# Optimization experiments

Hardware: AMD Instinct MI355X
Metric: run time of the kernel (lower is better)

The kernel has to match this reference:

```python
import jax, jax.numpy as jnp
import numpy as np
from jax import lax

PATCH = 16          # patch_size
LAM = 0.5           # lambda_sparse
TAU = 10.0          # tau
ITERS = 50          # lca_iterations
DT = 0.1            # LCA step size
N_BASES = 256
INPUT_DIM = PATCH * PATCH * 3


def setup_inputs() -> dict:
    key = jax.random.key(0)
    k1, k2 = jax.random.split(key)
    image = jax.random.normal(k1, (64, 3, 224, 224), dtype=jnp.float32)
    D = jax.random.normal(k2, (N_BASES, INPUT_DIM), dtype=jnp.float32)
    D = D / jnp.linalg.norm(D, axis=1, keepdims=True)  # unit-norm bases
    return {"image": image, "dictionary": D, "stride": 8}


def _softshrink(u):
    return jnp.sign(u) * jnp.maximum(jnp.abs(u) - LAM, 0.0)


def reference(image, dictionary, stride):
    n_bases = dictionary.shape[0]
    # extract overlapping patches, feature order (C, ph, pw) matches torch unfold layout
    patches = lax.conv_general_dilated_patches(
        image, (PATCH, PATCH), (stride, stride), 'VALID')  # (B, C*P*P, nh, nw)
    B, D, nh, nw = patches.shape
    patches = patches.transpose(0, 2, 3, 1).reshape(B, nh * nw, D)
    # per-patch standardization (torch .std is unbiased -> ddof=1)
    patches = patches - patches.mean(axis=-1, keepdims=True)
    std = jnp.std(patches, axis=-1, ddof=1, keepdims=True)
    patches = patches / (std + 1e-8)

    pf = patches.reshape(-1, D)  # (B*n_patches, input_dim)
    gram = dictionary @ dictionary.T - jnp.eye(n_bases, dtype=dictionary.dtype)
    b = pf @ dictionary.T        # (N, n_bases) feedforward drive

    def step(u, _):
        a = _softshrink(u)
        du = (b - u - a @ gram) / TAU
        return u + DT * du, None

    u0 = jnp.zeros_like(b)
    u, _ = lax.scan(step, u0, None, length=ITERS)
    codes = _softshrink(u).reshape(B, nh * nw, n_bases)
    return codes.max(axis=1)  # pool='max' -> (B, n_bases)
```

## Files before the change

kernel.cpp:

```cpp
#include <hip/hip_runtime.h>
#include <hip/hip_bf16.h>

#define NB 256
#define IDIM 768
#define NPP 729
#define PSTRIDE 768
#define NIMG 64
#define ITERS 50
#define LN 64
#define LBLK 12

typedef float f32x4 __attribute__((ext_vector_type(4)));
typedef short bf16x8 __attribute__((ext_vector_type(8)));

__device__ __forceinline__ short f2bf(float x) {
  union { float f; unsigned u; } v; v.f = x;
  unsigned r = v.u + 0x7FFFu + ((v.u >> 16) & 1u);
  return (short)(r >> 16);
}

__device__ __forceinline__ unsigned cvt_pk_bf16(float lo, float hi) {
  unsigned r;
  asm("v_cvt_pk_bf16_f32 %0, %1, %2" : "=v"(r) : "v"(lo), "v"(hi));
  return r;
}

__global__ __launch_bounds__(256) void k_cvt(const float* __restrict__ D,
                                             short* __restrict__ Dbf) {
  size_t i = (size_t)(blockIdx.x * 256 + threadIdx.x) * 8;
  float4 a = *(const float4*)(D + i);
  float4 b = *(const float4*)(D + i + 4);
  union { uint4 u4; bf16x8 v; } cv;
  cv.u4.x = cvt_pk_bf16(a.x, a.y); cv.u4.y = cvt_pk_bf16(a.z, a.w);
  cv.u4.z = cvt_pk_bf16(b.x, b.y); cv.u4.w = cvt_pk_bf16(b.z, b.w);
  *(bf16x8*)(Dbf + i) = cv.v;
}

__global__ __launch_bounds__(256) void k_gram(const short* __restrict__ Dbf,
                                              short* __restrict__ gram) {
  int r0 = blockIdx.x * 16;
  int t = threadIdx.x, w = t >> 6, l = t & 63, lr = l & 15, q = l >> 4;
  f32x4 acc[4];
  #pragma unroll
  for (int c = 0; c < 4; ++c) acc[c] = (f32x4){0.f, 0.f, 0.f, 0.f};
  for (int kc = 0; kc < 24; ++kc) {
    int k = kc * 32 + q * 8;
    bf16x8 a = *(const bf16x8*)(Dbf + (size_t)(r0 + lr) * IDIM + k);
    #pragma unroll
    for (int c = 0; c < 4; ++c) {
      int col = (w * 4 + c) * 16 + lr;
      bf16x8 b = *(const bf16x8*)(Dbf + (size_t)col * IDIM + k);
      acc[c] = __builtin_amdgcn_mfma_f32_16x16x32_bf16(a, b, acc[c], 0, 0, 0);
    }
  }
  #pragma unroll
  for (int c = 0; c < 4; ++c)
    #pragma unroll
    for (int r = 0; r < 4; ++r) {
      int row = r0 + q * 4 + r, col = (w * 4 + c) * 16 + lr;
      gram[row * NB + col] = f2bf(acc[c][r] - (row == col ? 1.f : 0.f));
    }
}

__global__ __launch_bounds__(256) void k_patches(const float* __restrict__ img,
                                                 const short* __restrict__ Dbf,
                                                 float* __restrict__ bbufT) {
  __shared__ float strip[3 * 16 * 224];
  __shared__ float s_mean[32], s_inv[32];
  int py = blockIdx.x, im = blockIdx.y;
  int t = threadIdx.x;

  for (int i = t; i < 2688; i += 256) {
    int c = i / 896, rem = i - c * 896, ph = rem / 56, x = rem - ph * 56;
    float4 v = *(const float4*)(img + ((size_t)(im * 3 + c)) * 50176 +
                                (size_t)(py * 8 + ph) * 224 + x * 4);
    *(float4*)(strip + (c * 16 + ph) * 224 + x * 4) = v;
  }
  __syncthreads();
  if (t < 216) {
    int p = t >> 3, s = t & 7;
    float sum = 0.f, ss = 0.f;
    for (int c = 0; c < 3; ++c)
      #pragma unroll
      for (int ph = 0; ph < 16; ++ph) {
        const float* rw = strip + (c * 16 + ph) * 224 + p * 8 + s * 2;
        float v0 = rw[0], v1 = rw[1];
        sum += v0 + v1; ss += v0 * v0 + v1 * v1;
      }
    #pragma unroll
    for (int d = 1; d < 8; d <<= 1) { sum += __shfl_xor(sum, d); ss += __shfl_xor(ss, d); }
    if (s == 0) {
      float mean = sum * (1.f / 768.f);
      float var = (ss - sum * mean) * (1.f / 767.f);
      float sd = sqrtf(fmaxf(var, 0.f));
      s_mean[p] = mean; s_inv[p] = 1.f / (sd + 1e-8f);
    }
  }
  __syncthreads();

  int w = t >> 6, l = t & 63, lr = l & 15, q = l >> 4;
  f32x4 acc[2][4];
  #pragma unroll
  for (int mi = 0; mi < 2; ++mi)
    #pragma unroll
    for (int c = 0; c < 4; ++c) acc[mi][c] = (f32x4){0.f, 0.f, 0.f, 0.f};

  for (int kc = 0; kc < 24; ++kc) {
    int k = kc * 32 + q * 8;
    int c = k >> 8, ph = (k >> 4) & 15, pw0 = k & 15;
    const float* rb = strip + (c * 16 + ph) * 224 + pw0;
    bf16x8 af[2];
    #pragma unroll
    for (int mi = 0; mi < 2; ++mi) {
      int patch = mi * 16 + lr;
      int px = patch < 27 ? patch : 26;
      const float* sp = rb + px * 8;
      float mn = s_mean[patch < 27 ? patch : 26], iv = s_inv[patch < 27 ? patch : 26];
      float4 v0 = *(const float4*)(sp);
      float4 v1 = *(const float4*)(sp + 4);
      union { uint4 u4; bf16x8 v; } cv;
      cv.u4.x = cvt_pk_bf16((v0.x - mn) * iv, (v0.y - mn) * iv);
      cv.u4.y = cvt_pk_bf16((v0.z - mn) * iv, (v0.w - mn) * iv);
      cv.u4.z = cvt_pk_bf16((v1.x - mn) * iv, (v1.y - mn) * iv);
      cv.u4.w = cvt_pk_bf16((v1.z - mn) * iv, (v1.w - mn) * iv);
      af[mi] = cv.v;
    }
    bf16x8 bfr[4];
    #pragma unroll
    for (int c4 = 0; c4 < 4; ++c4) {
      int col = (w * 4 + c4) * 16 + lr;
      bfr[c4] = *(const bf16x8*)(Dbf + (size_t)col * IDIM + k);
    }
    #pragma unroll
    for (int mi = 0; mi < 2; ++mi)
      #pragma unroll
      for (int c4 = 0; c4 < 4; ++c4)
        acc[mi][c4] = __builtin_amdgcn_mfma_f32_16x16x32_bf16(af[mi], bfr[c4], acc[mi][c4], 0, 0, 0);
  }

  int prow0 = py * 27;
  #pragma unroll
  for (int mi = 0; mi < 2; ++mi)
    #pragma unroll
    for (int c4 = 0; c4 < 4; ++c4) {
      int col = (w * 4 + c4) * 16 + lr;
      size_t base = ((size_t)(im * NB + col)) * PSTRIDE + prow0;
      #pragma unroll
      for (int r = 0; r < 4; ++r) {
        int patch = mi * 16 + q * 4 + r;
        if (patch < 27) bbufT[base + patch] = acc[mi][c4][r];
      }
    }
}

__global__ __launch_bounds__(512, 2) void k_lca(const float* __restrict__ bbufT,
                                                const short* __restrict__ gram,
                                                float* __restrict__ partial) {
  __shared__ char albuf[2][LN * 512];
  int blk = blockIdx.x, im = blockIdx.y;
  int t = threadIdx.x, w = t >> 6, l = t & 63, lr = l & 15, q = l >> 4;
  int p0 = blk * LN;
  int basew = w * 32;

  bf16x8 gA[2][8];
  #pragma unroll
  for (int mi = 0; mi < 2; ++mi)
    #pragma unroll
    for (int kc = 0; kc < 8; ++kc)
      gA[mi][kc] = *(const bf16x8*)(gram + (size_t)(basew + mi * 16 + lr) * NB + kc * 32 + q * 8);

  float u[2][4][4];
  int2 bpk[2][4];
  #pragma unroll
  for (int mi = 0; mi < 2; ++mi) {
    int basis0 = basew + mi * 16 + q * 4;
    #pragma unroll
    for (int nt = 0; nt < 4; ++nt) {
      int patch = nt * 16 + lr;
      size_t ga = ((size_t)(im * NB + basis0)) * PSTRIDE + p0 + patch;
      float b0 = bbufT[ga] * 0.01f;
      float b1 = bbufT[ga + PSTRIDE] * 0.01f;
      float b2 = bbufT[ga + 2 * PSTRIDE] * 0.01f;
      float b3 = bbufT[ga + 3 * PSTRIDE] * 0.01f;
      int2 pk = make_int2((int)cvt_pk_bf16(b0, b1), (int)cvt_pk_bf16(b2, b3));
      bpk[mi][nt] = pk;
      u[mi][nt][0] = __uint_as_float((unsigned)pk.x << 16);
      u[mi][nt][1] = __uint_as_float((unsigned)pk.x & 0xffff0000u);
      u[mi][nt][2] = __uint_as_float((unsigned)pk.y << 16);
      u[mi][nt][3] = __uint_as_float((unsigned)pk.y & 0xffff0000u);
    }
  }

  for (int it = 0; it < ITERS - 1; ++it) {
    char* abuf = albuf[it & 1];
    #pragma unroll
    for (int mi = 0; mi < 2; ++mi)
      #pragma unroll
      for (int nt = 0; nt < 4; ++nt) {
        int patch = nt * 16 + lr;
        float a0 = u[mi][nt][0] - __builtin_amdgcn_fmed3f(u[mi][nt][0], -0.5f, 0.5f);
        float a1 = u[mi][nt][1] - __builtin_amdgcn_fmed3f(u[mi][nt][1], -0.5f, 0.5f);
        float a2 = u[mi][nt][2] - __builtin_amdgcn_fmed3f(u[mi][nt][2], -0.5f, 0.5f);
        float a3 = u[mi][nt][3] - __builtin_amdgcn_fmed3f(u[mi][nt][3], -0.5f, 0.5f);
        int byte = (patch * 512 + basew * 2 + mi * 32 + q * 8) ^ ((patch & 7) << 4);
        *(int2*)(abuf + byte) = make_int2((int)cvt_pk_bf16(a0, a1), (int)cvt_pk_bf16(a2, a3));
      }
    __syncthreads();

    f32x4 acc[2][4];
    #pragma unroll
    for (int mi = 0; mi < 2; ++mi)
      #pragma unroll
      for (int nt = 0; nt < 4; ++nt) acc[mi][nt] = (f32x4){0.f, 0.f, 0.f, 0.f};
    #pragma unroll
    for (int kc = 0; kc < 8; ++kc) {
      bf16x8 ab[4];
      #pragma unroll
      for (int nt = 0; nt < 4; ++nt) {
        int patch = nt * 16 + lr;
        int byte = (patch * 512 + (kc * 32 + q * 8) * 2) ^ ((patch & 7) << 4);
        ab[nt] = *(const bf16x8*)(abuf + byte);
      }
      #pragma unroll
      for (int mi = 0; mi < 2; ++mi)
        #pragma unroll
        for (int nt = 0; nt < 4; ++nt)
          acc[mi][nt] = __builtin_amdgcn_mfma_f32_16x16x32_bf16(gA[mi][kc], ab[nt], acc[mi][nt], 0, 0, 0);
    }

    #pragma unroll
    for (int mi = 0; mi < 2; ++mi)
      #pragma unroll
      for (int nt = 0; nt < 4; ++nt) {
        int2 pk = bpk[mi][nt];
        float b0 = __uint_as_float((unsigned)pk.x << 16);
        float b1 = __uint_as_float((unsigned)pk.x & 0xffff0000u);
        float b2 = __uint_as_float((unsigned)pk.y << 16);
        float b3 = __uint_as_float((unsigned)pk.y & 0xffff0000u);
        u[mi][nt][0] = fmaf(0.99f, u[mi][nt][0], fmaf(-0.01f, acc[mi][nt][0], b0));
        u[mi][nt][1] = fmaf(0.99f, u[mi][nt][1], fmaf(-0.01f, acc[mi][nt][1], b1));
        u[mi][nt][2] = fmaf(0.99f, u[mi][nt][2], fmaf(-0.01f, acc[mi][nt][2], b2));
        u[mi][nt][3] = fmaf(0.99f, u[mi][nt][3], fmaf(-0.01f, acc[mi][nt][3], b3));
      }
  }

  #pragma unroll
  for (int mi = 0; mi < 2; ++mi)
    #pragma unroll
    for (int r = 0; r < 4; ++r) {
      float m = -3.402823466e38f;
      #pragma unroll
      for (int nt = 0; nt < 4; ++nt) {
        int patch = p0 + nt * 16 + lr;
        float uu = u[mi][nt][r];
        float a = uu - __builtin_amdgcn_fmed3f(uu, -0.5f, 0.5f);
        if (patch < NPP) m = fmaxf(m, a);
      }
      m = fmaxf(m, __shfl_xor(m, 1));
      m = fmaxf(m, __shfl_xor(m, 2));
      m = fmaxf(m, __shfl_xor(m, 4));
      m = fmaxf(m, __shfl_xor(m, 8));
      if (lr == 0)
        partial[(size_t)(im * LBLK + blk) * NB + basew + mi * 16 + q * 4 + r] = m;
    }
}

__global__ __launch_bounds__(256) void k_pool(const float* __restrict__ partial,
                                              float* __restrict__ out) {
  int im = blockIdx.x, n = threadIdx.x;
  float m = partial[(size_t)(im * LBLK) * NB + n];
  for (int b = 1; b < LBLK; ++b)
    m = fmaxf(m, partial[(size_t)(im * LBLK + b) * NB + n]);
  out[im * NB + n] = m;
}

extern "C" void kernel_launch(void* const* d_in, const int* in_sizes, int n_in,
                              void* d_out, int out_size, void* d_ws, size_t ws_size,
                              hipStream_t stream) {
  const float* img = (const float*)d_in[0];
  const float* D   = (const float*)d_in[1];

  char* ws = (char*)d_ws;
  short* gram    = (short*)(ws);
  short* Dbf     = (short*)(ws + 131072);
  float* bbufT   = (float*)(ws + 524288);
  float* partial = (float*)(ws + 50855936);
  float* out = (float*)d_out;

  hipLaunchKernelGGL(k_cvt, dim3(96), dim3(256), 0, stream, D, Dbf);
  hipLaunchKernelGGL(k_gram, dim3(16), dim3(256), 0, stream, Dbf, gram);
  hipLaunchKernelGGL(k_patches, dim3(27, NIMG), dim3(256), 0, stream, img, Dbf, bbufT);
  hipLaunchKernelGGL(k_lca, dim3(LBLK, NIMG), dim3(512), 0, stream, bbufT, gram, partial);
  hipLaunchKernelGGL(k_pool, dim3(NIMG), dim3(256), 0, stream, partial, out);
}
```

Before: 434.3 us.

## Fold patch normalization into GEMM epilogue and retile LCA waves 4x2

Patch standardization is moved out of the GEMM inner loop: raw pixels go to bf16, and the output is corrected as (acc - mean*sum(D_j)) * inv_std, with a new kernel precomputing the dictionary row sums. Separately, the LCA kernel is retiled so each wave owns 64 bases by 32 patches instead of 32 by 64. This keeps more gram fragments in registers and needs a shared-memory exchange to combine max-pool partials across the two patch halves. Quantizing raw (unnormalized) pixels to bf16 and then subtracting a large mean term may cost accuracy, and the retiling raises register pressure.

```diff
diff --git a/kernel.cpp b/kernel.cpp
--- a/kernel.cpp
+++ b/kernel.cpp
@@ -17,6 +17,10 @@
   union { float f; unsigned u; } v; v.f = x;
   unsigned r = v.u + 0x7FFFu + ((v.u >> 16) & 1u);
   return (short)(r >> 16);
+}
+
+__device__ __forceinline__ float bf2f(short s) {
+  return __uint_as_float((unsigned)(unsigned short)s << 16);
 }
 
 __device__ __forceinline__ unsigned cvt_pk_bf16(float lo, float hi) {
@@ -36,6 +40,18 @@
   *(bf16x8*)(Dbf + i) = cv.v;
 }
 
+__global__ __launch_bounds__(256) void k_dsum(const short* __restrict__ Dbf,
+                                              float* __restrict__ dsum) {
+  int j = threadIdx.x;
+  float s = 0.f;
+  for (int kc = 0; kc < 96; ++kc) {
+    bf16x8 v = *(const bf16x8*)(Dbf + (size_t)j * IDIM + kc * 8);
+    #pragma unroll
+    for (int i = 0; i < 8; ++i) s += bf2f(v[i]);
+  }
+  dsum[j] = s;
+}
+
 __global__ __launch_bounds__(256) void k_gram(const short* __restrict__ Dbf,
                                               short* __restrict__ gram) {
   int r0 = blockIdx.x * 16;
@@ -64,6 +80,7 @@
 
 __global__ __launch_bounds__(256) void k_patches(const float* __restrict__ img,
                                                  const short* __restrict__ Dbf,
+                                                 const float* __restrict__ dsum,
                                                  float* __restrict__ bbufT) {
   __shared__ float strip[3 * 16 * 224];
   __shared__ float s_mean[32], s_inv[32];
@@ -76,6 +93,7 @@
                                 (size_t)(py * 8 + ph) * 224 + x * 4);
     *(float4*)(strip + (c * 16 + ph) * 224 + x * 4) = v;
   }
+  if (t >= 216 && t < 221) { s_mean[27 + t - 216] = 0.f; s_inv[27 + t - 216] = 0.f; }
   __syncthreads();
   if (t < 216) {
     int p = t >> 3, s = t & 7;
@@ -115,14 +133,13 @@
       int patch = mi * 16 + lr;
       int px = patch < 27 ? patch : 26;
       const float* sp = rb + px * 8;
-      float mn = s_mean[patch < 27 ? patch : 26], iv = s_inv[patch < 27 ? patch : 26];
       float4 v0 = *(const float4*)(sp);
       float4 v1 = *(const float4*)(sp + 4);
       union { uint4 u4; bf16x8 v; } cv;
-      cv.u4.x = cvt_pk_bf16((v0.x - mn) * iv, (v0.y - mn) * iv);
-      cv.u4.y = cvt_pk_bf16((v0.z - mn) * iv, (v0.w - mn) * iv);
-      cv.u4.z = cvt_pk_bf16((v1.x - mn) * iv, (v1.y - mn) * iv);
-      cv.u4.w = cvt_pk_bf16((v1.z - mn) * iv, (v1.w - mn) * iv);
+      cv.u4.x = cvt_pk_bf16(v0.x, v0.y);
+      cv.u4.y = cvt_pk_bf16(v0.z, v0.w);
+      cv.u4.z = cvt_pk_bf16(v1.x, v1.y);
+      cv.u4.w = cvt_pk_bf16(v1.z, v1.w);
       af[mi] = cv.v;
     }
     bf16x8 bfr[4];
@@ -144,11 +161,15 @@
     #pragma unroll
     for (int c4 = 0; c4 < 4; ++c4) {
       int col = (w * 4 + c4) * 16 + lr;
+      float dsv = dsum[col];
       size_t base = ((size_t)(im * NB + col)) * PSTRIDE + prow0;
       #pragma unroll
       for (int r = 0; r < 4; ++r) {
         int patch = mi * 16 + q * 4 + r;
-        if (patch < 27) bbufT[base + patch] = acc[mi][c4][r];
+        if (patch < 27) {
+          float bv = (acc[mi][c4][r] - s_mean[patch] * dsv) * s_inv[patch];
+          bbufT[base + patch] = bv;
+        }
       }
     }
 }
@@ -159,24 +180,26 @@
   __shared__ char albuf[2][LN * 512];
   int blk = blockIdx.x, im = blockIdx.y;
   int t = threadIdx.x, w = t >> 6, l = t & 63, lr = l & 15, q = l >> 4;
+  int wm = w >> 1, wn = w & 1;
   int p0 = blk * LN;
-  int basew = w * 32;
-
-  bf16x8 gA[2][8];
-  #pragma unroll
-  for (int mi = 0; mi < 2; ++mi)
+  int basew = wm * 64;
+  int pw = wn * 32;
+
+  bf16x8 gA[4][8];
+  #pragma unroll
+  for (int mi = 0; mi < 4; ++mi)
     #pragma unroll
     for (int kc = 0; kc < 8; ++kc)
       gA[mi][kc] = *(const bf16x8*)(gram + (size_t)(basew + mi * 16 + lr) * NB + kc * 32 + q * 8);
 
-  float u[2][4][4];
-  int2 bpk[2][4];
-  #pragma unroll
-  for (int mi = 0; mi < 2; ++mi) {
+  float u[4][2][4];
+  int2 bpk[4][2];
+  #pragma unroll
+  for (int mi = 0; mi < 4; ++mi) {
     int basis0 = basew + mi * 16 + q * 4;
     #pragma unroll
-    for (int nt = 0; nt < 4; ++nt) {
-      int patch = nt * 16 + lr;
+    for (int nt = 0; nt < 2; ++nt) {
+      int patch = pw + nt * 16 + lr;
       size_t ga = ((size_t)(im * NB + basis0)) * PSTRIDE + p0 + patch;
       float b0 = bbufT[ga] * 0.01f;
       float b1 = bbufT[ga + PSTRIDE] * 0.01f;
@@ -194,44 +217,44 @@
   for (int it = 0; it < ITERS - 1; ++it) {
     char* abuf = albuf[it & 1];
     #pragma unroll
-    for (int mi = 0; mi < 2; ++mi)
-      #pragma unroll
-      for (int nt = 0; nt < 4; ++nt) {
-        int patch = nt * 16 + lr;
+    for (int mi = 0; mi < 4; ++mi)
+      #pragma unroll
+      for (int nt = 0; nt < 2; ++nt) {
+        int patch = pw + nt * 16 + lr;
         float a0 = u[mi][nt][0] - __builtin_amdgcn_fmed3f(u[mi][nt][0], -0.5f, 0.5f);
         float a1 = u[mi][nt][1] - __builtin_amdgcn_fmed3f(u[mi][nt][1], -0.5f, 0.5f);
         float a2 = u[mi][nt][2] - __builtin_amdgcn_fmed3f(u[mi][nt][2], -0.5f, 0.5f);
         float a3 = u[mi][nt][3] - __builtin_amdgcn_fmed3f(u[mi][nt][3], -0.5f, 0.5f);
-        int byte = (patch * 512 + basew * 2 + mi * 32 + q * 8) ^ ((patch & 7) << 4);
+        int byte = (patch * 512 + (basew + mi * 16 + q * 4) * 2) ^ ((patch & 7) << 4);
         *(int2*)(abuf + byte) = make_int2((int)cvt_pk_bf16(a0, a1), (int)cvt_pk_bf16(a2, a3));
       }
     __syncthreads();
 
-    f32x4 acc[2][4];
-    #pragma unroll
-    for (int mi = 0; mi < 2; ++mi)
-      #pragma unroll
-      for (int nt = 0; nt < 4; ++nt) acc[mi][nt] = (f32x4){0.f, 0.f, 0.f, 0.f};
+    f32x4 acc[4][2];
+    #pragma unroll
+    for (int mi = 0; mi < 4; ++mi)
+      #pragma unroll
+      for (int nt = 0; nt < 2; ++nt) acc[mi][nt] = (f32x4){0.f, 0.f, 0.f, 0.f};
     #pragma unroll
     for (int kc = 0; kc < 8; ++kc) {
-      bf16x8 ab[4];
-      #pragma unroll
-      for (int nt = 0; nt < 4; ++nt) {
-        int patch = nt * 16 + lr;
+      bf16x8 ab[2];
+      #pragma unroll
+      for (int nt = 0; nt < 2; ++nt) {
+        int patch = pw + nt * 16 + lr;
         int byte = (patch * 512 + (kc * 32 + q * 8) * 2) ^ ((patch & 7) << 4);
         ab[nt] = *(const bf16x8*)(abuf + byte);
       }
       #pragma unroll
-      for (int mi = 0; mi < 2; ++mi)
+      for (int mi = 0; mi < 4; ++mi)
         #pragma unroll
-        for (int nt = 0; nt < 4; ++nt)
+        for (int nt = 0; nt < 2; ++nt)
           acc[mi][nt] = __builtin_amdgcn_mfma_f32_16x16x32_bf16(gA[mi][kc], ab[nt], acc[mi][nt], 0, 0, 0);
     }
 
     #pragma unroll
-    for (int mi = 0; mi < 2; ++mi)
-      #pragma unroll
-      for (int nt = 0; nt < 4; ++nt) {
+    for (int mi = 0; mi < 4; ++mi)
+      #pragma unroll
+      for (int nt = 0; nt < 2; ++nt) {
         int2 pk = bpk[mi][nt];
         float b0 = __uint_as_float((unsigned)pk.x << 16);
         float b1 = __uint_as_float((unsigned)pk.x & 0xffff0000u);
@@ -244,14 +267,15 @@
       }
   }
 
-  #pragma unroll
-  for (int mi = 0; mi < 2; ++mi)
+  float mred[4][4];
+  #pragma unroll
+  for (int mi = 0; mi < 4; ++mi)
     #pragma unroll
     for (int r = 0; r < 4; ++r) {
       float m = -3.402823466e38f;
       #pragma unroll
-      for (int nt = 0; nt < 4; ++nt) {
-        int patch = p0 + nt * 16 + lr;
+      for (int nt = 0; nt < 2; ++nt) {
+        int patch = p0 + pw + nt * 16 + lr;
         float uu = u[mi][nt][r];
         float a = uu - __builtin_amdgcn_fmed3f(uu, -0.5f, 0.5f);
         if (patch < NPP) m = fmaxf(m, a);
@@ -260,9 +284,29 @@
       m = fmaxf(m, __shfl_xor(m, 2));
       m = fmaxf(m, __shfl_xor(m, 4));
       m = fmaxf(m, __shfl_xor(m, 8));
-      if (lr == 0)
-        partial[(size_t)(im * LBLK + blk) * NB + basew + mi * 16 + q * 4 + r] = m;
-    }
+      mred[mi][r] = m;
+    }
+
+  float* xch = (float*)albuf;
+  __syncthreads();
+  if (wn == 1 && lr == 0) {
+    #pragma unroll
+    for (int mi = 0; mi < 4; ++mi)
+      #pragma unroll
+      for (int r = 0; r < 4; ++r)
+        xch[basew + mi * 16 + q * 4 + r] = mred[mi][r];
+  }
+  __syncthreads();
+  if (wn == 0 && lr == 0) {
+    #pragma unroll
+    for (int mi = 0; mi < 4; ++mi)
+      #pragma unroll
+      for (int r = 0; r < 4; ++r) {
+        int basis = basew + mi * 16 + q * 4 + r;
+        float m = fmaxf(mred[mi][r], xch[basis]);
+        partial[(size_t)(im * LBLK + blk) * NB + basis] = m;
+      }
+  }
 }
 
 __global__ __launch_bounds__(256) void k_pool(const float* __restrict__ partial,
@@ -283,13 +327,15 @@
   char* ws = (char*)d_ws;
   short* gram    = (short*)(ws);
   short* Dbf     = (short*)(ws + 131072);
-  float* bbufT   = (float*)(ws + 524288);
-  float* partial = (float*)(ws + 50855936);
+  float* dsum    = (float*)(ws + 524288);
+  float* bbufT   = (float*)(ws + 528384);
+  float* partial = (float*)(ws + 50860032);
   float* out = (float*)d_out;
 
   hipLaunchKernelGGL(k_cvt, dim3(96), dim3(256), 0, stream, D, Dbf);
+  hipLaunchKernelGGL(k_dsum, dim3(1), dim3(256), 0, stream, Dbf, dsum);
   hipLaunchKernelGGL(k_gram, dim3(16), dim3(256), 0, stream, Dbf, gram);
-  hipLaunchKernelGGL(k_patches, dim3(27, NIMG), dim3(256), 0, stream, img, Dbf, bbufT);
+  hipLaunchKernelGGL(k_patches, dim3(27, NIMG), dim3(256), 0, stream, img, Dbf, dsum, bbufT);
   hipLaunchKernelGGL(k_lca, dim3(LBLK, NIMG), dim3(512), 0, stream, bbufT, gram, partial);
   hipLaunchKernelGGL(k_pool, dim3(NIMG), dim3(256), 0, stream, partial, out);
 }
```

New measurement: 450.8 us. 1.04x slower.
